# Performance work log

Measured on AMD Instinct MI355X. Metric: run time of the kernel, lower is better.

The kernel has to match this reference:

```python
import jax, jax.numpy as jnp
import numpy as np

NUM_TIMESCALES = 16
MAX_TIME = 100.0
N_HEADS = 4
MLP_WIDTH = 128
HIDDEN_EACH = 128  # hidden_size // attn_n_heads = 512 // 4


def setup_inputs() -> dict:
    key = jax.random.key(0)
    ks = jax.random.split(key, 8)
    B, ROWS_PER_PAT, V = 32, 64, 32
    R = B * ROWS_PER_PAT
    # patient i has counts[i] observations, laid out row-major in its block of rows
    counts = 512 + 16 * np.arange(B)
    M = np.zeros((R, V), np.int32)
    for i in range(B):
        flat = M[i * ROWS_PER_PAT:(i + 1) * ROWS_PER_PAT].reshape(-1)
        flat[:counts[i]] = 1
    n_obs = int(counts.sum())        # 24320
    max_n_obs = int(counts.max())    # 1008
    n_in = 2 * NUM_TIMESCALES + 2    # 34

    def lin(k, o, i_):
        kw, kb = jax.random.split(k)
        return (jax.random.normal(kw, (o, i_)) * (1.0 / np.sqrt(i_)),
                jax.random.normal(kb, (o,)) * 0.01)

    W0, b0 = lin(ks[0], MLP_WIDTH, n_in)
    W1, b1 = lin(ks[1], MLP_WIDTH, MLP_WIDTH)
    W2, b2 = lin(ks[2], HIDDEN_EACH, MLP_WIDTH)
    Wq, bq = lin(ks[3], HIDDEN_EACH, HIDDEN_EACH)
    Wk, bk = lin(ks[4], HIDDEN_EACH, HIDDEN_EACH)
    return {
        "times": jax.random.uniform(ks[5], (R,)) * MAX_TIME,
        "time_ptr": jnp.arange(R + 1),
        "X": jax.random.normal(ks[6], (R, V)),
        "M": jnp.asarray(M),
        "obs_idx": jnp.repeat(jnp.arange(B), ROWS_PER_PAT),
        "pat_idx": jnp.arange(B),
        "W0": W0, "b0": b0, "W1": W1, "b1": b1, "W2": W2, "b2": b2,
        "Wq": Wq, "bq": bq, "Wk": Wk, "bk": bk,
        "n_obs": n_obs, "max_n_obs": max_n_obs,
    }


def reference(times, time_ptr, X, M, obs_idx, pat_idx,
              W0, b0, W1, b1, W2, b2, Wq, bq, Wk, bk, n_obs, max_n_obs):
    B = pat_idx.shape[0]
    # --- ragged scatter: (time_row, var) observations -> padded per-patient sets ---
    rows, cols = jnp.nonzero(M, size=n_obs)          # row-major, grouped by patient
    p = obs_idx[rows]                                # patient id per observation
    vals = X[rows, cols]
    t_arr = jnp.repeat(times, jnp.diff(time_ptr), total_repeat_length=X.shape[0])
    t = t_arr[rows]
    lens = jnp.bincount(p, length=B)
    starts = jnp.cumsum(lens) - lens
    pos = jnp.arange(n_obs) - starts[p]              # within-patient slot index
    Sv = jnp.zeros((B, max_n_obs), X.dtype).at[p, pos].set(cols.astype(X.dtype))
    Sx = jnp.zeros((B, max_n_obs), X.dtype).at[p, pos].set(vals)
    St = jnp.zeros((B, max_n_obs), X.dtype).at[p, pos].set(t)
    pad = jnp.arange(max_n_obs)[None, :] >= lens[:, None]   # True = padding
    # --- time embedding + feature concat: [sin, cos, var, value] ---
    timescales = MAX_TIME ** jnp.linspace(0.0, 1.0, NUM_TIMESCALES)
    st = St[..., None] / timescales
    new_X = jnp.concatenate([jnp.sin(st), jnp.cos(st), Sv[..., None], Sx[..., None]], axis=-1)
    # --- encoder MLP (depth 3 -> 1 hidden layer, eval mode: dropout is identity) ---
    h = jax.nn.relu(new_X @ W0.T + b0)
    h = jax.nn.relu(h @ W1.T + b1)
    enc = h @ W2.T + b2                              # [B, L, 128]
    # --- masked self-attention weights (only q/k matter; output is discarded) ---
    L = max_n_obs
    hd = HIDDEN_EACH // N_HEADS
    q = (enc @ Wq.T + bq).reshape(B, L, N_HEADS, hd)
    k = (enc @ Wk.T + bk).reshape(B, L, N_HEADS, hd)
    scores = jnp.einsum('blhd,bmhd->bhlm', q, k) / np.sqrt(hd)
    scores = jnp.where(pad[:, None, None, :], -1e30, scores)
    attn = jax.nn.softmax(scores, axis=-1)           # [B, H, L, L]
    w = attn[:, :, -1, :]                            # last-query attention row
    summed = jnp.einsum('bhl,ble->bhe', w, enc)      # [B, H, 128]
    return summed.reshape(B, -1)                     # [B, 512]
```

## Files before the change

### kernel.cpp

```cpp
#include <hip/hip_runtime.h>

#define B_PAT 32
#define RTOT 2048
#define NV 32
#define LMAX 1008
#define NTS 16
#define NIN 64
#define TLD 72
#define HW 128
#define LDSP 136
#define NCH 16
#define CH 63
#define ELD 132
#define RLD 136

typedef __attribute__((ext_vector_type(8))) short short8;
typedef __attribute__((ext_vector_type(4))) float floatx4;

__device__ __forceinline__ ushort f2b(float f) {
  unsigned int x = __float_as_uint(f);
  unsigned int r = (x + 0x7FFFu + ((x >> 16) & 1u)) >> 16;
  return (ushort)r;
}
__device__ __forceinline__ unsigned int pack2(ushort lo, ushort hi) {
  return (unsigned int)lo | ((unsigned int)hi << 16);
}
__device__ __forceinline__ float tscale(int i) {
  return exp2f((float)i * (6.643856189774724f / 15.0f));
}

__global__ __launch_bounds__(256) void kP(
    const float* __restrict__ times, const int* __restrict__ time_ptr,
    const float* __restrict__ X, const int* __restrict__ M,
    const int* __restrict__ obs_idx,
    const float* __restrict__ W0, const float* __restrict__ b0,
    const float* __restrict__ W1, const float* __restrict__ b1,
    const float* __restrict__ W2, const float* __restrict__ b2,
    const float* __restrict__ Wq, const float* __restrict__ bq,
    const float* __restrict__ Wk,
    int* __restrict__ pbase_g, int* __restrict__ rowstart_g,
    int* __restrict__ lens, float* __restrict__ trow_g,
    ushort* __restrict__ W0p, ushort* __restrict__ W1b, ushort* __restrict__ W2b,
    float* __restrict__ r_all)
{
  const int b = blockIdx.x;
  const int t = threadIdx.x;
  if (b >= B_PAT) {
    if (b == B_PAT) {
      for (int i = t; i < HW * NIN; i += 256) {
        int n = i >> 6, k = i & 63;
        W0p[i] = (k < 34) ? f2b(W0[n * 34 + k]) : (ushort)0;
      }
    } else if (b == B_PAT + 1) {
      for (int i = t; i < HW * HW; i += 256) W1b[i] = f2b(W1[i]);
    } else {
      for (int i = t; i < HW * HW; i += 256) W2b[i] = f2b(W2[i]);
    }
    return;
  }
  __shared__ int rs_s, re_s;
  __shared__ int cnt_s[64];
  __shared__ int pbase_s[65];
  __shared__ float tval_s[64];
  __shared__ int qrc[3];
  __shared__ float x_s[64];
  __shared__ float h0[HW], h1[HW], eq[HW], q_s[HW], part[256];
  for (int r = t * 8; r < t * 8 + 8; ++r) {
    if (obs_idx[r] == b) {
      if (r == 0 || obs_idx[r - 1] != b) rs_s = r;
      if (r == RTOT - 1 || obs_idx[r + 1] != b) re_s = r + 1;
    }
  }
  __syncthreads();
  const int rs = rs_s, re = re_s;
  const int n = re - rs;
  if (t < 64) {
    int c = 0;
    if (t < n) {
      const int4* mp = (const int4*)(M + (size_t)(rs + t) * NV);
#pragma unroll
      for (int q = 0; q < 8; ++q) {
        int4 m4 = mp[q];
        c += (m4.x != 0) + (m4.y != 0) + (m4.z != 0) + (m4.w != 0);
      }
      int lo = 0, hi = RTOT - 1, r = rs + t;
      while (lo < hi) { int mid = (lo + hi + 1) >> 1; if (time_ptr[mid] <= r) lo = mid; else hi = mid - 1; }
      tval_s[t] = times[lo];
      trow_g[r] = times[lo];
    }
    cnt_s[t] = c;
  }
  __syncthreads();
  if (t < 64) {
    int incl = cnt_s[t];
    for (int off = 1; off < 64; off <<= 1) {
      int v = __shfl_up(incl, off);
      if (t >= off) incl += v;
    }
    pbase_s[t + 1] = incl;
    if (t == 0) pbase_s[0] = 0;
  }
  __syncthreads();
  const int len = pbase_s[64];
  if (t < 65) pbase_g[b * 65 + t] = pbase_s[t];
  if (t == 0) { rowstart_g[b] = rs; lens[b] = len; }
  if (t == 0) {
    if (LMAX - 1 < len) {
      int lr = 0;
      while (pbase_s[lr + 1] <= LMAX - 1) ++lr;
      int k = (LMAX - 1) - pbase_s[lr], col = 0;
      for (int cc = 0; cc < NV; ++cc)
        if (M[(size_t)(rs + lr) * NV + cc] != 0) { if (k == 0) { col = cc; break; } --k; }
      qrc[0] = lr; qrc[1] = col; qrc[2] = 1;
    } else qrc[2] = 0;
  }
  if (t < 64) x_s[t] = 0.0f;
  __syncthreads();
  if (qrc[2] == 0) {
    if (t >= 16 && t < 32) x_s[t] = 1.0f;
  } else {
    int lr = qrc[0], col = qrc[1];
    if (t < 16) {
      float a = tval_s[lr] / tscale(t);
      x_s[t] = sinf(a); x_s[16 + t] = cosf(a);
    }
    if (t == 0) { x_s[32] = (float)col; x_s[33] = X[(size_t)(rs + lr) * NV + col]; }
  }
  __syncthreads();
  if (t < HW) {
    float a = b0[t];
#pragma unroll 2
    for (int k = 0; k < 34; ++k) a += W0[t * 34 + k] * x_s[k];
    h0[t] = fmaxf(a, 0.0f);
  }
  __syncthreads();
  {
    int oo = t & 127, hf = t >> 7;
    float a = 0.f;
    const float* wr = W1 + oo * HW + hf * 64;
#pragma unroll 8
    for (int k = 0; k < 64; ++k) a += wr[k] * h0[hf * 64 + k];
    part[t] = a;
  }
  __syncthreads();
  if (t < HW) h1[t] = fmaxf(part[t] + part[t + 128] + b1[t], 0.0f);
  __syncthreads();
  {
    int oo = t & 127, hf = t >> 7;
    float a = 0.f;
    const float* wr = W2 + oo * HW + hf * 64;
#pragma unroll 8
    for (int k = 0; k < 64; ++k) a += wr[k] * h1[hf * 64 + k];
    part[t] = a;
  }
  __syncthreads();
  if (t < HW) eq[t] = part[t] + part[t + 128] + b2[t];
  __syncthreads();
  {
    int oo = t & 127, hf = t >> 7;
    float a = 0.f;
    const float* wr = Wq + oo * HW + hf * 64;
#pragma unroll 8
    for (int k = 0; k < 64; ++k) a += wr[k] * eq[hf * 64 + k];
    part[t] = a;
  }
  __syncthreads();
  if (t < HW) q_s[t] = part[t] + part[t + 128] + bq[t];
  __syncthreads();
  const float scale = 0.17677669529663687f;
  for (int idx = t; idx < 512; idx += 256) {
    int h = idx >> 7, e = idx & 127;
    float a = 0.f;
#pragma unroll 8
    for (int d = 0; d < 32; ++d) a += Wk[(h * 32 + d) * HW + e] * q_s[h * 32 + d];
    r_all[b * 512 + idx] = a * scale;
  }
}

__global__ __launch_bounds__(256) void kF(
    const int* __restrict__ M, const float* __restrict__ X,
    const int* __restrict__ pbase_g, const int* __restrict__ rowstart_g,
    const int* __restrict__ lens, const float* __restrict__ trow_g,
    const ushort* __restrict__ W0p, const float* __restrict__ b0,
    const ushort* __restrict__ W1b, const float* __restrict__ b1,
    const ushort* __restrict__ W2b, const float* __restrict__ b2,
    const float* __restrict__ r_all, float* __restrict__ partial,
    float2* __restrict__ mxsm)
{
  const int bx = blockIdx.x;
  const int b = bx >> 4, c = bx & 15;
  const int t = threadIdx.x;
  const int len = lens[b];
  const int start = c * CH;
  int valid = len - start; if (valid > CH) valid = CH;
  if (valid <= 0) {
    if (t < 4) mxsm[bx * 4 + t] = make_float2(-1e30f, 0.0f);
    return;
  }
  __shared__ ushort tile[64 * TLD];
  __shared__ ushort bufA[64 * LDSP];
  __shared__ ushort bufB[64 * LDSP];
  __shared__ float encs[64 * ELD];
  __shared__ float r_s[4 * RLD];
  __shared__ float lg[4 * 64];
  __shared__ unsigned int umask[64];
  __shared__ float tval[64];
  __shared__ int pbase_s[65];
  __shared__ float inv_ts[NTS];
  __shared__ float mx_s[4], sm_s[4];
  const int rs = rowstart_g[b];
  {
    uint4 z = make_uint4(0u, 0u, 0u, 0u);
    uint4* tp = (uint4*)tile;
    for (int i = t; i < 64 * TLD / 8; i += 256) tp[i] = z;
    for (int i = t; i < 512; i += 256)
      r_s[(i >> 7) * RLD + (i & 127)] = r_all[b * 512 + i];
  }
  if (t < 64) {
    int r = rs + t;
    unsigned int mk = 0;
    const int* mp = M + (size_t)r * NV;
#pragma unroll
    for (int cc = 0; cc < NV; ++cc) mk |= (mp[cc] != 0 ? 1u : 0u) << cc;
    umask[t] = mk;
    tval[t] = trow_g[r];
  } else if (t < 129) {
    pbase_s[t - 64] = pbase_g[b * 65 + (t - 64)];
  } else if (t >= 136 && t < 136 + NTS) {
    inv_ts[t - 136] = 1.0f / tscale(t - 136);
  }
  __syncthreads();
  {
    int pos = t >> 2, sub = t & 3;
    if (pos < valid) {
      int gpos = start + pos;
      int lo = 0, hi = 63;
      while (lo < hi) { int mid = (lo + hi + 1) >> 1; if (pbase_s[mid] <= gpos) lo = mid; else hi = mid - 1; }
      int lrow = lo;
      int rank = gpos - pbase_s[lrow];
      unsigned int m = umask[lrow];
      for (int i = 0; i < rank; ++i) m &= m - 1;
      int col = (m != 0u) ? __builtin_ctz(m) : 0;
      float tv = tval[lrow];
      unsigned int* dst = (unsigned int*)(tile + pos * TLD);
      if (sub == 0) {
#pragma unroll
        for (int w = 0; w < 8; ++w)
          dst[w] = pack2(f2b(sinf(tv * inv_ts[2 * w])), f2b(sinf(tv * inv_ts[2 * w + 1])));
      } else if (sub == 1) {
#pragma unroll
        for (int w = 0; w < 8; ++w)
          dst[8 + w] = pack2(f2b(cosf(tv * inv_ts[2 * w])), f2b(cosf(tv * inv_ts[2 * w + 1])));
      } else if (sub == 2) {
        dst[16] = pack2(f2b((float)col), f2b(X[(size_t)(rs + lrow) * NV + col]));
      }
    }
  }
  __syncthreads();
  const int wv = t >> 6, lane = t & 63;
  const int m16 = lane & 15, quad = lane >> 4;
  const int rowl = wv * 16 + m16;
  {
    const short8* ar = (const short8*)(tile + rowl * TLD);
    short8 a0 = ar[quad];
    short8 a1 = ar[4 + quad];
#pragma unroll
    for (int nt = 0; nt < 8; ++nt) {
      int nn = nt * 16 + m16;
      const short8* br = (const short8*)(W0p + nn * NIN);
      floatx4 acc = {0.f, 0.f, 0.f, 0.f};
      acc = __builtin_amdgcn_mfma_f32_16x16x32_bf16(a0, br[quad], acc, 0, 0, 0);
      acc = __builtin_amdgcn_mfma_f32_16x16x32_bf16(a1, br[4 + quad], acc, 0, 0, 0);
      float bias = b0[nn];
#pragma unroll
      for (int i = 0; i < 4; ++i) {
        float vv = fmaxf(acc[i] + bias, 0.0f);
        bufA[(wv * 16 + quad * 4 + i) * LDSP + nn] = f2b(vv);
      }
    }
  }
  __syncthreads();
  {
#pragma unroll
    for (int nt = 0; nt < 8; ++nt) {
      int nn = nt * 16 + m16;
      floatx4 acc = {0.f, 0.f, 0.f, 0.f};
#pragma unroll
      for (int ks = 0; ks < 4; ++ks) {
        short8 a = *(const short8*)(bufA + rowl * LDSP + ks * 32 + quad * 8);
        short8 bb = *(const short8*)(W1b + nn * HW + ks * 32 + quad * 8);
        acc = __builtin_amdgcn_mfma_f32_16x16x32_bf16(a, bb, acc, 0, 0, 0);
      }
      float bias = b1[nn];
#pragma unroll
      for (int i = 0; i < 4; ++i) {
        float vv = fmaxf(acc[i] + bias, 0.0f);
        bufB[(wv * 16 + quad * 4 + i) * LDSP + nn] = f2b(vv);
      }
    }
  }
  __syncthreads();
  {
#pragma unroll
    for (int nt = 0; nt < 8; ++nt) {
      int nn = nt * 16 + m16;
      floatx4 acc = {0.f, 0.f, 0.f, 0.f};
#pragma unroll
      for (int ks = 0; ks < 4; ++ks) {
        short8 a = *(const short8*)(bufB + rowl * LDSP + ks * 32 + quad * 8);
        short8 bb = *(const short8*)(W2b + nn * HW + ks * 32 + quad * 8);
        acc = __builtin_amdgcn_mfma_f32_16x16x32_bf16(a, bb, acc, 0, 0, 0);
      }
      float bias = b2[nn];
#pragma unroll
      for (int i = 0; i < 4; ++i)
        encs[(wv * 16 + quad * 4 + i) * ELD + nn] = acc[i] + bias;
    }
  }
  __syncthreads();
  {
    int m = t >> 2, h = t & 3;
    if (m < valid) {
      const float4* ev = (const float4*)(&encs[m * ELD]);
      const float4* rv = (const float4*)(&r_s[h * RLD]);
      float acc = 0.f;
#pragma unroll
      for (int e4 = 0; e4 < 32; ++e4) {
        float4 v = ev[e4], r = rv[e4];
        acc += v.x * r.x + v.y * r.y + v.z * r.z + v.w * r.w;
      }
      lg[h * 64 + m] = acc;
    }
  }
  __syncthreads();
  {
    float v = (lane < valid) ? lg[wv * 64 + lane] : -1e30f;
    float mx = v;
#pragma unroll
    for (int o = 32; o >= 1; o >>= 1) mx = fmaxf(mx, __shfl_xor(mx, o));
    float p = (lane < valid) ? expf(v - mx) : 0.f;
    lg[wv * 64 + lane] = p;
    float sm = p;
#pragma unroll
    for (int o = 32; o >= 1; o >>= 1) sm += __shfl_xor(sm, o);
    if (lane == 0) { mx_s[wv] = mx; sm_s[wv] = sm; }
  }
  __syncthreads();
  for (int idx = t; idx < 512; idx += 256) {
    int h = idx >> 7, e = idx & 127;
    float acc = 0.f;
    for (int m = 0; m < valid; ++m)
      acc += lg[h * 64 + m] * encs[m * ELD + e];
    partial[(size_t)bx * 512 + idx] = acc;
  }
  if (t < 4) mxsm[bx * 4 + t] = make_float2(mx_s[t], sm_s[t]);
}

__global__ __launch_bounds__(256) void kK(
    const float* __restrict__ partial, const float2* __restrict__ mxsm,
    float* __restrict__ out)
{
  const int b = blockIdx.x;
  const int tid = threadIdx.x;
  __shared__ float f_s[NCH * 4];
  if (tid < 4) {
    int h = tid;
    float2 v[NCH];
    float M = -1e30f;
#pragma unroll
    for (int c = 0; c < NCH; ++c) {
      v[c] = mxsm[(b * NCH + c) * 4 + h];
      if (v[c].y > 0.f) M = fmaxf(M, v[c].x);
    }
    float S = 0.f;
#pragma unroll
    for (int c = 0; c < NCH; ++c)
      if (v[c].y > 0.f) S += v[c].y * expf(v[c].x - M);
    float invS = 1.0f / S;
#pragma unroll
    for (int c = 0; c < NCH; ++c)
      f_s[c * 4 + h] = (v[c].y > 0.f) ? expf(v[c].x - M) * invS : 0.f;
  }
  __syncthreads();
  for (int idx = tid; idx < 512; idx += 256) {
    int h = idx >> 7;
    float acc = 0.f;
#pragma unroll
    for (int c = 0; c < NCH; ++c) {
      float f = f_s[c * 4 + h];
      if (f > 0.f) acc += partial[((size_t)(b * NCH + c)) * 512 + idx] * f;
    }
    out[b * 512 + idx] = acc;
  }
}

extern "C" void kernel_launch(void* const* d_in, const int* in_sizes, int n_in,
                              void* d_out, int out_size, void* d_ws, size_t ws_size,
                              hipStream_t stream) {
  const float* times = (const float*)d_in[0];
  const int* time_ptr = (const int*)d_in[1];
  const float* X = (const float*)d_in[2];
  const int* M = (const int*)d_in[3];
  const int* obs_idx = (const int*)d_in[4];
  const float* W0 = (const float*)d_in[6];
  const float* b0 = (const float*)d_in[7];
  const float* W1 = (const float*)d_in[8];
  const float* b1 = (const float*)d_in[9];
  const float* W2 = (const float*)d_in[10];
  const float* b2 = (const float*)d_in[11];
  const float* Wq = (const float*)d_in[12];
  const float* bq = (const float*)d_in[13];
  const float* Wk = (const float*)d_in[14];
  float* out = (float*)d_out;

  char* ws = (char*)d_ws;
  size_t off = 0;
  int* pbase_g = (int*)(ws + off); off += (size_t)B_PAT * 65 * 4;
  int* rowstart_g = (int*)(ws + off); off += 256;
  int* lens = (int*)(ws + off); off += 256;
  float* trow_g = (float*)(ws + off); off += RTOT * 4;
  ushort* W0p = (ushort*)(ws + off); off += (size_t)HW * NIN * 2;
  ushort* W1b = (ushort*)(ws + off); off += (size_t)HW * HW * 2;
  ushort* W2b = (ushort*)(ws + off); off += (size_t)HW * HW * 2;
  float* r_all = (float*)(ws + off); off += (size_t)B_PAT * 512 * 4;
  float* partial = (float*)(ws + off); off += (size_t)B_PAT * NCH * 512 * 4;
  float2* mxsm = (float2*)(ws + off); off += (size_t)B_PAT * NCH * 4 * 8;

  kP<<<B_PAT + 3, 256, 0, stream>>>(times, time_ptr, X, M, obs_idx,
                                    W0, b0, W1, b1, W2, b2, Wq, bq, Wk,
                                    pbase_g, rowstart_g, lens, trow_g,
                                    W0p, W1b, W2b, r_all);
  kF<<<B_PAT * NCH, 256, 0, stream>>>(M, X, pbase_g, rowstart_g, lens, trow_g,
                                      W0p, b0, W1b, b1, W2b, b2, r_all,
                                      partial, mxsm);
  kK<<<B_PAT, 256, 0, stream>>>(partial, mxsm, out);
}
```

Baseline: 147.2 us.

## Double kF block to 512 threads, split MLP output columns across waves

Launches the fused kernel with 512 threads per block and splits each MLP layer's 128 output columns into two halves handled by separate wave groups. The feature build and logit stages are respread over more threads. The mask row is now read as int4 vectors, and the fast __sinf/__cosf/__expf intrinsics replace the precise ones. The aim is to cut per-block latency across the 512 small blocks, at the cost of lower precision in the time embedding and softmax and possibly fewer resident blocks per CU.

```diff
diff --git a/kernel.cpp b/kernel.cpp
--- a/kernel.cpp
+++ b/kernel.cpp
@@ -177,7 +177,7 @@
   }
 }
 
-__global__ __launch_bounds__(256) void kF(
+__global__ __launch_bounds__(512) void kF(
     const int* __restrict__ M, const float* __restrict__ X,
     const int* __restrict__ pbase_g, const int* __restrict__ rowstart_g,
     const int* __restrict__ lens, const float* __restrict__ trow_g,
@@ -212,18 +212,22 @@
   {
     uint4 z = make_uint4(0u, 0u, 0u, 0u);
     uint4* tp = (uint4*)tile;
-    for (int i = t; i < 64 * TLD / 8; i += 256) tp[i] = z;
-    for (int i = t; i < 512; i += 256)
-      r_s[(i >> 7) * RLD + (i & 127)] = r_all[b * 512 + i];
+    for (int i = t; i < 64 * TLD / 8; i += 512) tp[i] = z;
+    if (t < 512) r_s[(t >> 7) * RLD + (t & 127)] = r_all[b * 512 + t];
   }
   if (t < 64) {
-    int r = rs + t;
+    const int4* mp = (const int4*)(M + (size_t)(rs + t) * NV);
     unsigned int mk = 0;
-    const int* mp = M + (size_t)r * NV;
-#pragma unroll
-    for (int cc = 0; cc < NV; ++cc) mk |= (mp[cc] != 0 ? 1u : 0u) << cc;
+#pragma unroll
+    for (int q8 = 0; q8 < 8; ++q8) {
+      int4 m4 = mp[q8];
+      mk |= (m4.x != 0 ? 1u : 0u) << (q8 * 4);
+      mk |= (m4.y != 0 ? 1u : 0u) << (q8 * 4 + 1);
+      mk |= (m4.z != 0 ? 1u : 0u) << (q8 * 4 + 2);
+      mk |= (m4.w != 0 ? 1u : 0u) << (q8 * 4 + 3);
+    }
     umask[t] = mk;
-    tval[t] = trow_g[r];
+    tval[t] = trow_g[rs + t];
   } else if (t < 129) {
     pbase_s[t - 64] = pbase_g[b * 65 + (t - 64)];
   } else if (t >= 136 && t < 136 + NTS) {
@@ -231,8 +235,8 @@
   }
   __syncthreads();
   {
-    int pos = t >> 2, sub = t & 3;
-    if (pos < valid) {
+    int pos = t >> 3, sub = t & 7;
+    if (pos < valid && sub < 5) {
       int gpos = start + pos;
       int lo = 0, hi = 63;
       while (lo < hi) { int mid = (lo + hi + 1) >> 1; if (pbase_s[mid] <= gpos) lo = mid; else hi = mid - 1; }
@@ -243,15 +247,19 @@
       int col = (m != 0u) ? __builtin_ctz(m) : 0;
       float tv = tval[lrow];
       unsigned int* dst = (unsigned int*)(tile + pos * TLD);
-      if (sub == 0) {
-#pragma unroll
-        for (int w = 0; w < 8; ++w)
-          dst[w] = pack2(f2b(sinf(tv * inv_ts[2 * w])), f2b(sinf(tv * inv_ts[2 * w + 1])));
-      } else if (sub == 1) {
-#pragma unroll
-        for (int w = 0; w < 8; ++w)
-          dst[8 + w] = pack2(f2b(cosf(tv * inv_ts[2 * w])), f2b(cosf(tv * inv_ts[2 * w + 1])));
-      } else if (sub == 2) {
+      if (sub < 2) {
+#pragma unroll
+        for (int w = 0; w < 4; ++w) {
+          int i0 = sub * 8 + 2 * w;
+          dst[sub * 4 + w] = pack2(f2b(__sinf(tv * inv_ts[i0])), f2b(__sinf(tv * inv_ts[i0 + 1])));
+        }
+      } else if (sub < 4) {
+#pragma unroll
+        for (int w = 0; w < 4; ++w) {
+          int i0 = (sub - 2) * 8 + 2 * w;
+          dst[8 + (sub - 2) * 4 + w] = pack2(f2b(__cosf(tv * inv_ts[i0])), f2b(__cosf(tv * inv_ts[i0 + 1])));
+        }
+      } else {
         dst[16] = pack2(f2b((float)col), f2b(X[(size_t)(rs + lrow) * NV + col]));
       }
     }
@@ -259,14 +267,15 @@
   __syncthreads();
   const int wv = t >> 6, lane = t & 63;
   const int m16 = lane & 15, quad = lane >> 4;
-  const int rowl = wv * 16 + m16;
+  const int rg = wv & 3, nh = wv >> 2;
+  const int rowl = rg * 16 + m16;
   {
     const short8* ar = (const short8*)(tile + rowl * TLD);
     short8 a0 = ar[quad];
     short8 a1 = ar[4 + quad];
 #pragma unroll
-    for (int nt = 0; nt < 8; ++nt) {
-      int nn = nt * 16 + m16;
+    for (int nt = 0; nt < 4; ++nt) {
+      int nn = nh * 64 + nt * 16 + m16;
       const short8* br = (const short8*)(W0p + nn * NIN);
       floatx4 acc = {0.f, 0.f, 0.f, 0.f};
       acc = __builtin_amdgcn_mfma_f32_16x16x32_bf16(a0, br[quad], acc, 0, 0, 0);
@@ -275,15 +284,15 @@
 #pragma unroll
       for (int i = 0; i < 4; ++i) {
         float vv = fmaxf(acc[i] + bias, 0.0f);
-        bufA[(wv * 16 + quad * 4 + i) * LDSP + nn] = f2b(vv);
-      }
-    }
-  }
-  __syncthreads();
-  {
-#pragma unroll
-    for (int nt = 0; nt < 8; ++nt) {
-      int nn = nt * 16 + m16;
+        bufA[(rg * 16 + quad * 4 + i) * LDSP + nn] = f2b(vv);
+      }
+    }
+  }
+  __syncthreads();
+  {
+#pragma unroll
+    for (int nt = 0; nt < 4; ++nt) {
+      int nn = nh * 64 + nt * 16 + m16;
       floatx4 acc = {0.f, 0.f, 0.f, 0.f};
 #pragma unroll
       for (int ks = 0; ks < 4; ++ks) {
@@ -295,15 +304,15 @@
 #pragma unroll
       for (int i = 0; i < 4; ++i) {
         float vv = fmaxf(acc[i] + bias, 0.0f);
-        bufB[(wv * 16 + quad * 4 + i) * LDSP + nn] = f2b(vv);
-      }
-    }
-  }
-  __syncthreads();
-  {
-#pragma unroll
-    for (int nt = 0; nt < 8; ++nt) {
-      int nn = nt * 16 + m16;
+        bufB[(rg * 16 + quad * 4 + i) * LDSP + nn] = f2b(vv);
+      }
+    }
+  }
+  __syncthreads();
+  {
+#pragma unroll
+    for (int nt = 0; nt < 4; ++nt) {
+      int nn = nh * 64 + nt * 16 + m16;
       floatx4 acc = {0.f, 0.f, 0.f, 0.f};
 #pragma unroll
       for (int ks = 0; ks < 4; ++ks) {
@@ -314,13 +323,13 @@
       float bias = b2[nn];
 #pragma unroll
       for (int i = 0; i < 4; ++i)
-        encs[(wv * 16 + quad * 4 + i) * ELD + nn] = acc[i] + bias;
-    }
-  }
-  __syncthreads();
-  {
-    int m = t >> 2, h = t & 3;
-    if (m < valid) {
+        encs[(rg * 16 + quad * 4 + i) * ELD + nn] = acc[i] + bias;
+    }
+  }
+  __syncthreads();
+  {
+    int m = t >> 3, h = t & 7;
+    if (m < valid && h < 4) {
       const float4* ev = (const float4*)(&encs[m * ELD]);
       const float4* rv = (const float4*)(&r_s[h * RLD]);
       float acc = 0.f;
@@ -333,12 +342,12 @@
     }
   }
   __syncthreads();
-  {
+  if (wv < 4) {
     float v = (lane < valid) ? lg[wv * 64 + lane] : -1e30f;
     float mx = v;
 #pragma unroll
     for (int o = 32; o >= 1; o >>= 1) mx = fmaxf(mx, __shfl_xor(mx, o));
-    float p = (lane < valid) ? expf(v - mx) : 0.f;
+    float p = (lane < valid) ? __expf(v - mx) : 0.f;
     lg[wv * 64 + lane] = p;
     float sm = p;
 #pragma unroll
@@ -346,12 +355,12 @@
     if (lane == 0) { mx_s[wv] = mx; sm_s[wv] = sm; }
   }
   __syncthreads();
-  for (int idx = t; idx < 512; idx += 256) {
-    int h = idx >> 7, e = idx & 127;
+  {
+    int h = t >> 7, e = t & 127;
     float acc = 0.f;
     for (int m = 0; m < valid; ++m)
       acc += lg[h * 64 + m] * encs[m * ELD + e];
-    partial[(size_t)bx * 512 + idx] = acc;
+    partial[(size_t)bx * 512 + t] = acc;
   }
   if (t < 4) mxsm[bx * 4 + t] = make_float2(mx_s[t], sm_s[t]);
 }
@@ -430,7 +439,7 @@
                                     W0, b0, W1, b1, W2, b2, Wq, bq, Wk,
                                     pbase_g, rowstart_g, lens, trow_g,
                                     W0p, W1b, W2b, r_all);
-  kF<<<B_PAT * NCH, 256, 0, stream>>>(M, X, pbase_g, rowstart_g, lens, trow_g,
+  kF<<<B_PAT * NCH, 512, 0, stream>>>(M, X, pbase_g, rowstart_g, lens, trow_g,
                                       W0p, b0, W1b, b1, W2b, b2, r_all,
                                       partial, mxsm);
   kK<<<B_PAT, 256, 0, stream>>>(partial, mxsm, out);
```

Result: faster. 141.0 us (-4.2%).
